# Optimization experiments

Hardware: AMD Instinct MI355X
Metric: run time of the kernel (lower is better)

The kernel has to match this reference:

```python
import jax, jax.numpy as jnp
import numpy as np

N = 100000   # nodes
E = 1600000  # edges
F = 64       # num_node_features
H = 48       # size_conv_layers
K = 5        # filter_size (Chebyshev order)
C = 2        # classes
EPS = 1e-5
SLOPE = 0.01  # LeakyReLU default negative_slope


def setup_inputs() -> dict:
    key = jax.random.key(0)
    ks = jax.random.split(key, 16)
    x = jax.random.normal(ks[0], (N, F), dtype=jnp.float32)
    edge_index = jax.random.randint(ks[1], (2, E), 0, N, dtype=jnp.int64)
    s = 0.1
    return {
        "x": x,
        "edge_index": edge_index,
        "W1": jax.random.normal(ks[2], (K, F, H), dtype=jnp.float32) * s,
        "b1": jnp.zeros((H,), jnp.float32),
        "W2": jax.random.normal(ks[3], (K, H, H), dtype=jnp.float32) * s,
        "b2": jnp.zeros((H,), jnp.float32),
        "W3": jax.random.normal(ks[4], (K, H, H), dtype=jnp.float32) * s,
        "b3": jnp.zeros((H,), jnp.float32),
        "g1": jnp.ones((H,), jnp.float32),
        "bt1": jnp.zeros((H,), jnp.float32),
        "g2": jnp.ones((H,), jnp.float32),
        "bt2": jnp.zeros((H,), jnp.float32),
        "Wf": jax.random.normal(ks[5], (H, C), dtype=jnp.float32) * s,
        "bf": jnp.zeros((C,), jnp.float32),
    }


def _cheb_norm(edge_index, n, dtype):
    # PyG ChebConv sym norm with lambda_max=2: L_hat = -D^-1/2 A D^-1/2 (zero diagonal)
    src, dst = edge_index[0], edge_index[1]
    deg = jax.ops.segment_sum(jnp.ones((edge_index.shape[1],), dtype), src, num_segments=n)
    dinv = jnp.where(deg > 0, jax.lax.rsqrt(jnp.maximum(deg, 1e-12)), 0.0)
    return -dinv[src] * dinv[dst], src, dst


def _cheb_conv(x, src, dst, norm, W, b, n):
    # Tx_0 = x; Tx_1 = L_hat x; Tx_k = 2 L_hat Tx_{k-1} - Tx_{k-2}
    def prop(t):
        return jax.ops.segment_sum(norm[:, None] * t[src], dst, num_segments=n)
    Tx0 = x
    out = Tx0 @ W[0]
    Tx1 = prop(Tx0)
    out = out + Tx1 @ W[1]
    for k in range(2, W.shape[0]):
        Tx2 = 2.0 * prop(Tx1) - Tx0
        out = out + Tx2 @ W[k]
        Tx0, Tx1 = Tx1, Tx2
    return out + b


def _bn_lrelu(x, g, b):
    mu = jnp.mean(x, axis=0)
    var = jnp.mean(jnp.square(x - mu), axis=0)  # biased var (train-mode BN)
    y = (x - mu) * jax.lax.rsqrt(var + EPS) * g + b
    return jnp.where(y >= 0, y, SLOPE * y)


def reference(x, edge_index, W1, b1, W2, b2, W3, b3, g1, bt1, g2, bt2, Wf, bf):
    n = x.shape[0]
    norm, src, dst = _cheb_norm(edge_index, n, x.dtype)
    h = _cheb_conv(x, src, dst, norm, W1, b1, n)
    h = _bn_lrelu(h, g1, bt1)
    h = _cheb_conv(h, src, dst, norm, W2, b2, n)
    h = _bn_lrelu(h, g2, bt2)
    h = _cheb_conv(h, src, dst, norm, W3, b3, n)  # no BN/act after last conv
    return h @ Wf + bf
```

## Files before the change

kernel.cpp:

```cpp
#include <hip/hip_runtime.h>

#define NHID 48
#define BN_EPS 1e-5f
#define SLOPE 0.01f
#define DMAX 64

typedef short short8 __attribute__((ext_vector_type(8)));
typedef float f32x4 __attribute__((ext_vector_type(4)));

__device__ __forceinline__ float bf_lo(unsigned u) { union { unsigned i; float f; } c; c.i = u << 16; return c.f; }
__device__ __forceinline__ float bf_hi(unsigned u) { union { unsigned i; float f; } c; c.i = u & 0xffff0000u; return c.f; }
__device__ __forceinline__ unsigned bf_rne(float x) { union { float f; unsigned i; } c; c.f = x; return (c.i + 0x7fffu + ((c.i >> 16) & 1u)) >> 16; }
__device__ __forceinline__ unsigned packbf(float lo, float hi) { return bf_rne(lo) | (bf_rne(hi) << 16); }

__device__ __forceinline__ void acc8(float (&a)[8], float w, const uint4& v) {
    a[0] = fmaf(w, bf_lo(v.x), a[0]); a[1] = fmaf(w, bf_hi(v.x), a[1]);
    a[2] = fmaf(w, bf_lo(v.y), a[2]); a[3] = fmaf(w, bf_hi(v.y), a[3]);
    a[4] = fmaf(w, bf_lo(v.z), a[4]); a[5] = fmaf(w, bf_hi(v.z), a[5]);
    a[6] = fmaf(w, bf_lo(v.w), a[6]); a[7] = fmaf(w, bf_hi(v.w), a[7]);
}

__global__ void k_setup(const int* __restrict__ src, const int* __restrict__ dst,
                        float* __restrict__ degf, int* __restrict__ cur,
                        int* __restrict__ csrc, int nE) {
    for (int e = blockIdx.x * blockDim.x + threadIdx.x; e < nE; e += gridDim.x * blockDim.x) {
        int s = src[e], d = dst[e];
        atomicAdd(&degf[s], 1.0f);
        int r = atomicAdd(&cur[d], 1);
        if (r < DMAX) csrc[(size_t)d * DMAX + r] = s;
    }
}

__global__ void k_dinv(float* __restrict__ deg, int nN) {
    for (int i = blockIdx.x * blockDim.x + threadIdx.x; i < nN; i += gridDim.x * blockDim.x) {
        float d = deg[i];
        deg[i] = (d > 0.f) ? rsqrtf(d) : 0.f;
    }
}

__global__ void k_cast(const float4* __restrict__ in, uint2* __restrict__ outv, int n4) {
    for (int i = blockIdx.x * blockDim.x + threadIdx.x; i < n4; i += gridDim.x * blockDim.x) {
        float4 v = in[i];
        outv[i] = make_uint2(packbf(v.x, v.y), packbf(v.z, v.w));
    }
}

template <int NV>
__global__ void k_prop(const uint4* __restrict__ Tin, const uint4* __restrict__ Tprev,
                       uint4* __restrict__ Tout, const int* __restrict__ cnt,
                       const int* __restrict__ csrc, const float* __restrict__ dinv,
                       int nN, int mode) {
    const int lane = threadIdx.x;
    const int x = lane & 7;
    const int y = lane >> 3;
    for (int n = blockIdx.x * 4 + threadIdx.y; n < nN; n += gridDim.x * 4) {
        int eb = n << 6;
        int c = cnt[n]; if (c > DMAX) c = DMAX;
        float a[8] = {0.f, 0.f, 0.f, 0.f, 0.f, 0.f, 0.f, 0.f};
        for (int it = 0; it < c; it += 16) {
            int j0 = it + y, j1 = it + 8 + y;
            int s0 = (j0 < c) ? csrc[eb + j0] : 0;
            int s1 = (j1 < c) ? csrc[eb + j1] : 0;
            float w0 = (j0 < c) ? dinv[s0] : 0.f;
            float w1 = (j1 < c) ? dinv[s1] : 0.f;
            if (x < NV) {
                uint4 q0 = Tin[(size_t)s0 * NV + x];
                uint4 q1 = Tin[(size_t)s1 * NV + x];
                acc8(a, w0, q0);
                acc8(a, w1, q1);
            }
        }
#pragma unroll
        for (int k = 0; k < 8; ++k) {
            float v = a[k];
            v += __shfl_xor(v, 8);
            v += __shfl_xor(v, 16);
            v += __shfl_xor(v, 32);
            a[k] = v;
        }
        if (y == 0 && x < NV) {
            float dn = -dinv[n];
            size_t o = (size_t)n * NV + x;
            uint4 r;
            if (mode) {
                uint4 p = Tprev[o];
                float t = 2.f * dn;
                r.x = packbf(fmaf(t, a[0], -bf_lo(p.x)), fmaf(t, a[1], -bf_hi(p.x)));
                r.y = packbf(fmaf(t, a[2], -bf_lo(p.y)), fmaf(t, a[3], -bf_hi(p.y)));
                r.z = packbf(fmaf(t, a[4], -bf_lo(p.z)), fmaf(t, a[5], -bf_hi(p.z)));
                r.w = packbf(fmaf(t, a[6], -bf_lo(p.w)), fmaf(t, a[7], -bf_hi(p.w)));
            } else {
                r.x = packbf(dn * a[0], dn * a[1]);
                r.y = packbf(dn * a[2], dn * a[3]);
                r.z = packbf(dn * a[4], dn * a[5]);
                r.w = packbf(dn * a[6], dn * a[7]);
            }
            Tout[o] = r;
        }
    }
}

template <int WIN, int MODE>
__global__ __launch_bounds__(256) void k_mmf(
    const unsigned short* __restrict__ Tslab, const float* __restrict__ Wb,
    const float* __restrict__ bias, unsigned short* __restrict__ Hout,
    float* __restrict__ bns, const float* __restrict__ Wf,
    const float* __restrict__ bfin, float* __restrict__ out, int nN) {
    constexpr int K = 5 * WIN;
    constexpr int NC = (K + 31) / 32;
    const int lane = threadIdx.x & 63;
    const int wid = threadIdx.x >> 6;
    const int col = lane & 15;
    const int sub = lane >> 4;
    const size_t termStride = (size_t)nN * WIN;

    short8 bfrag[3][NC];
#pragma unroll
    for (int ct = 0; ct < 3; ++ct) {
        int j = ct * 16 + col;
#pragma unroll
        for (int c = 0; c < NC; ++c) {
            short8 b;
#pragma unroll
            for (int r = 0; r < 8; ++r) {
                int k = c * 32 + sub * 8 + r;
                float w = (k < K) ? Wb[(size_t)k * 48 + j] : 0.f;
                b[r] = (short)bf_rne(w);
            }
            bfrag[ct][c] = b;
        }
    }
    float bj0 = bias[col], bj1 = bias[16 + col], bj2 = bias[32 + col];
    float wf00 = 0.f, wf01 = 0.f, wf02 = 0.f, wf10 = 0.f, wf11 = 0.f, wf12 = 0.f;
    float bf0 = 0.f, bf1 = 0.f;
    if (MODE == 1) {
        wf00 = Wf[(col) * 2 + 0];      wf10 = Wf[(col) * 2 + 1];
        wf01 = Wf[(16 + col) * 2 + 0]; wf11 = Wf[(16 + col) * 2 + 1];
        wf02 = Wf[(32 + col) * 2 + 0]; wf12 = Wf[(32 + col) * 2 + 1];
        bf0 = bfin[0]; bf1 = bfin[1];
    }
    float s0 = 0.f, s1 = 0.f, s2 = 0.f, q0 = 0.f, q1 = 0.f, q2 = 0.f;

    const int ntiles = (nN + 15) >> 4;
    for (int tile = blockIdx.x * 4 + wid; tile < ntiles; tile += gridDim.x * 4) {
        int n0 = tile << 4;
        int arow = n0 + col;
        bool rowok = arow < nN;
        f32x4 acc0 = {0.f, 0.f, 0.f, 0.f};
        f32x4 acc1 = {0.f, 0.f, 0.f, 0.f};
        f32x4 acc2 = {0.f, 0.f, 0.f, 0.f};
#pragma unroll
        for (int c = 0; c < NC; ++c) {
            int k = c * 32 + sub * 8;
            short8 a = {};
            if (rowok && k < K) {
                int t = k / WIN, f = k % WIN;
                a = *(const short8*)(Tslab + (size_t)t * termStride + (size_t)arow * WIN + f);
            }
            acc0 = __builtin_amdgcn_mfma_f32_16x16x32_bf16(a, bfrag[0][c], acc0, 0, 0, 0);
            acc1 = __builtin_amdgcn_mfma_f32_16x16x32_bf16(a, bfrag[1][c], acc1, 0, 0, 0);
            acc2 = __builtin_amdgcn_mfma_f32_16x16x32_bf16(a, bfrag[2][c], acc2, 0, 0, 0);
        }
        int nb = n0 + sub * 4;
        if (MODE == 0) {
#pragma unroll
            for (int r = 0; r < 4; ++r) {
                int n = nb + r;
                if (n < nN) {
                    float v0 = acc0[r] + bj0;
                    float v1 = acc1[r] + bj1;
                    float v2 = acc2[r] + bj2;
                    size_t ro = (size_t)n * NHID;
                    Hout[ro + col]      = (unsigned short)bf_rne(v0);
                    Hout[ro + 16 + col] = (unsigned short)bf_rne(v1);
                    Hout[ro + 32 + col] = (unsigned short)bf_rne(v2);
                    s0 += v0; q0 += v0 * v0;
                    s1 += v1; q1 += v1 * v1;
                    s2 += v2; q2 += v2 * v2;
                }
            }
        } else {
#pragma unroll
            for (int r = 0; r < 4; ++r) {
                float p0 = fmaf(acc0[r] + bj0, wf00, fmaf(acc1[r] + bj1, wf01, (acc2[r] + bj2) * wf02));
                float p1 = fmaf(acc0[r] + bj0, wf10, fmaf(acc1[r] + bj1, wf11, (acc2[r] + bj2) * wf12));
                p0 += __shfl_xor(p0, 1); p0 += __shfl_xor(p0, 2);
                p0 += __shfl_xor(p0, 4); p0 += __shfl_xor(p0, 8);
                p1 += __shfl_xor(p1, 1); p1 += __shfl_xor(p1, 2);
                p1 += __shfl_xor(p1, 4); p1 += __shfl_xor(p1, 8);
                int n = nb + r;
                if (col == 0 && n < nN) {
                    out[(size_t)n * 2 + 0] = p0 + bf0;
                    out[(size_t)n * 2 + 1] = p1 + bf1;
                }
            }
        }
    }
    if (MODE == 0) {
        s0 += __shfl_xor(s0, 16); s0 += __shfl_xor(s0, 32);
        s1 += __shfl_xor(s1, 16); s1 += __shfl_xor(s1, 32);
        s2 += __shfl_xor(s2, 16); s2 += __shfl_xor(s2, 32);
        q0 += __shfl_xor(q0, 16); q0 += __shfl_xor(q0, 32);
        q1 += __shfl_xor(q1, 16); q1 += __shfl_xor(q1, 32);
        q2 += __shfl_xor(q2, 16); q2 += __shfl_xor(q2, 32);
        __shared__ float red[4][96];
        if (lane < 16) {
            red[wid][col]      = s0; red[wid][16 + col] = s1; red[wid][32 + col] = s2;
            red[wid][48 + col] = q0; red[wid][64 + col] = q1; red[wid][80 + col] = q2;
        }
        __syncthreads();
        int t = threadIdx.x;
        if (t < 96) atomicAdd(&bns[t], red[0][t] + red[1][t] + red[2][t] + red[3][t]);
    }
}

__global__ void k_bn_apply(const unsigned short* __restrict__ Hin, unsigned short* __restrict__ T0,
                           const float* __restrict__ sums, const float* __restrict__ g,
                           const float* __restrict__ b, int nN) {
    int col = threadIdx.x;
    float inv = 1.f / (float)nN;
    float mu = sums[col] * inv;
    float var = sums[NHID + col] * inv - mu * mu;
    float rs = rsqrtf(var + BN_EPS) * g[col];
    float bb = b[col];
    for (int n = blockIdx.x * 8 + threadIdx.y; n < nN; n += gridDim.x * 8) {
        size_t o = (size_t)n * NHID + col;
        float y = (bf_lo(Hin[o]) - mu) * rs + bb;
        y = (y >= 0.f) ? y : SLOPE * y;
        T0[o] = (unsigned short)bf_rne(y);
    }
}

extern "C" void kernel_launch(void* const* d_in, const int* in_sizes, int n_in,
                              void* d_out, int out_size, void* d_ws, size_t ws_size,
                              hipStream_t stream) {
    const float* x   = (const float*)d_in[0];
    const int*   ei  = (const int*)d_in[1];
    const float* W1  = (const float*)d_in[2];
    const float* b1  = (const float*)d_in[3];
    const float* W2  = (const float*)d_in[4];
    const float* b2  = (const float*)d_in[5];
    const float* W3  = (const float*)d_in[6];
    const float* b3  = (const float*)d_in[7];
    const float* g1  = (const float*)d_in[8];
    const float* bt1 = (const float*)d_in[9];
    const float* g2  = (const float*)d_in[10];
    const float* bt2 = (const float*)d_in[11];
    const float* Wf  = (const float*)d_in[12];
    const float* bf  = (const float*)d_in[13];
    float* out = (float*)d_out;

    const int nN = in_sizes[0] / 64;
    const int nE = in_sizes[1] / 2;
    const int* src = ei;
    const int* dst = ei + nE;

    size_t off = 0;
    auto carve = [&](size_t bytes) -> void* {
        void* p = (char*)d_ws + off;
        off += (bytes + 255) & ~(size_t)255;
        return p;
    };
    float*          dinv = (float*)carve((size_t)nN * 4);
    int*            cur  = (int*)carve((size_t)nN * 4);
    int*            csrc = (int*)carve((size_t)nN * DMAX * 4);
    unsigned short* slab = (unsigned short*)carve((size_t)nN * 64 * 2 * 5);
    unsigned short* H    = (unsigned short*)carve((size_t)nN * NHID * 2);
    float*          bns  = (float*)carve(2 * NHID * 4);

    const size_t ts64 = (size_t)nN * 64;
    const size_t ts48 = (size_t)nN * NHID;

    hipMemsetAsync(dinv, 0, (size_t)nN * 4, stream);
    hipMemsetAsync(cur, 0, (size_t)nN * 4, stream);

    k_setup<<<4096, 256, 0, stream>>>(src, dst, dinv, cur, csrc, nE);
    k_dinv<<<1024, 256, 0, stream>>>(dinv, nN);
    k_cast<<<2048, 256, 0, stream>>>((const float4*)x, (uint2*)slab, nN * 16);

    const int gP = 2048;
    const dim3 blkP(64, 4);
    const int gM = 512;

    auto prop = [&](const unsigned short* Tin, const unsigned short* Tprev,
                    unsigned short* Tout, int NVw, int mode) {
        if (NVw == 8)
            k_prop<8><<<gP, blkP, 0, stream>>>((const uint4*)Tin, (const uint4*)Tprev,
                                               (uint4*)Tout, cur, csrc, dinv, nN, mode);
        else
            k_prop<6><<<gP, blkP, 0, stream>>>((const uint4*)Tin, (const uint4*)Tprev,
                                               (uint4*)Tout, cur, csrc, dinv, nN, mode);
    };

    unsigned short* L1[5];
    for (int t = 0; t < 5; ++t) L1[t] = slab + t * ts64;
    prop(L1[0], nullptr, L1[1], 8, 0);
    prop(L1[1], L1[0], L1[2], 8, 1);
    prop(L1[2], L1[1], L1[3], 8, 1);
    prop(L1[3], L1[2], L1[4], 8, 1);
    hipMemsetAsync(bns, 0, 2 * NHID * 4, stream);
    k_mmf<64, 0><<<gM, 256, 0, stream>>>(slab, W1, b1, H, bns, nullptr, nullptr, nullptr, nN);
    k_bn_apply<<<1024, dim3(NHID, 8), 0, stream>>>(H, slab, bns, g1, bt1, nN);

    unsigned short* L2[5];
    for (int t = 0; t < 5; ++t) L2[t] = slab + t * ts48;
    prop(L2[0], nullptr, L2[1], 6, 0);
    prop(L2[1], L2[0], L2[2], 6, 1);
    prop(L2[2], L2[1], L2[3], 6, 1);
    prop(L2[3], L2[2], L2[4], 6, 1);
    hipMemsetAsync(bns, 0, 2 * NHID * 4, stream);
    k_mmf<48, 0><<<gM, 256, 0, stream>>>(slab, W2, b2, H, bns, nullptr, nullptr, nullptr, nN);
    k_bn_apply<<<1024, dim3(NHID, 8), 0, stream>>>(H, slab, bns, g2, bt2, nN);

    prop(L2[0], nullptr, L2[1], 6, 0);
    prop(L2[1], L2[0], L2[2], 6, 1);
    prop(L2[2], L2[1], L2[3], 6, 1);
    prop(L2[3], L2[2], L2[4], 6, 1);
    k_mmf<48, 1><<<gM, 256, 0, stream>>>(slab, W3, b3, nullptr, nullptr, Wf, bf, out, nN);
}
```

Baseline: 813.9 us.

## Split feature slabs into 16-wide panels and propagate panel by panel

Stores each Chebyshev term as separate 16-feature panels (node-major within a panel) instead of full-width rows, and rewrites propagation to loop over panels, each edge gather reading 32 bytes per node from a smaller, more cache-resident panel. Matmul and BN-apply kernels are adapted to read and write the paneled layout, and the dinv and cast kernels are merged into one. The goal is better L2 locality for random neighbor gathers, at the cost of re-reading the CSR and dinv once per panel and using more shuffle reductions.

```diff
diff --git a/kernel.cpp b/kernel.cpp
--- a/kernel.cpp
+++ b/kernel.cpp
@@ -31,71 +31,75 @@
     }
 }
 
-__global__ void k_dinv(float* __restrict__ deg, int nN) {
-    for (int i = blockIdx.x * blockDim.x + threadIdx.x; i < nN; i += gridDim.x * blockDim.x) {
+__global__ void k_dinvcast(float* __restrict__ deg, int nN,
+                           const float4* __restrict__ xin, uint2* __restrict__ outv, int n4) {
+    int stride = gridDim.x * blockDim.x;
+    int gid = blockIdx.x * blockDim.x + threadIdx.x;
+    for (int i = gid; i < n4; i += stride) {
+        float4 v = xin[i];
+        int n = i >> 4, q = i & 15;
+        int p = q >> 2, w = q & 3;
+        outv[((size_t)p * nN + n) * 4 + w] = make_uint2(packbf(v.x, v.y), packbf(v.z, v.w));
+    }
+    for (int i = gid; i < nN; i += stride) {
         float d = deg[i];
         deg[i] = (d > 0.f) ? rsqrtf(d) : 0.f;
     }
 }
 
-__global__ void k_cast(const float4* __restrict__ in, uint2* __restrict__ outv, int n4) {
-    for (int i = blockIdx.x * blockDim.x + threadIdx.x; i < n4; i += gridDim.x * blockDim.x) {
-        float4 v = in[i];
-        outv[i] = make_uint2(packbf(v.x, v.y), packbf(v.z, v.w));
-    }
-}
-
-template <int NV>
-__global__ void k_prop(const uint4* __restrict__ Tin, const uint4* __restrict__ Tprev,
-                       uint4* __restrict__ Tout, const int* __restrict__ cnt,
-                       const int* __restrict__ csrc, const float* __restrict__ dinv,
-                       int nN, int mode) {
+__global__ void k_propP(const unsigned short* __restrict__ Tin,
+                        const unsigned short* __restrict__ Tprev,
+                        unsigned short* __restrict__ Tout,
+                        const int* __restrict__ cnt, const int* __restrict__ csrc,
+                        const float* __restrict__ dinv, int nN, int NP, int mode) {
     const int lane = threadIdx.x;
-    const int x = lane & 7;
-    const int y = lane >> 3;
-    for (int n = blockIdx.x * 4 + threadIdx.y; n < nN; n += gridDim.x * 4) {
-        int eb = n << 6;
-        int c = cnt[n]; if (c > DMAX) c = DMAX;
-        float a[8] = {0.f, 0.f, 0.f, 0.f, 0.f, 0.f, 0.f, 0.f};
-        for (int it = 0; it < c; it += 16) {
-            int j0 = it + y, j1 = it + 8 + y;
-            int s0 = (j0 < c) ? csrc[eb + j0] : 0;
-            int s1 = (j1 < c) ? csrc[eb + j1] : 0;
-            float w0 = (j0 < c) ? dinv[s0] : 0.f;
-            float w1 = (j1 < c) ? dinv[s1] : 0.f;
-            if (x < NV) {
-                uint4 q0 = Tin[(size_t)s0 * NV + x];
-                uint4 q1 = Tin[(size_t)s1 * NV + x];
-                acc8(a, w0, q0);
-                acc8(a, w1, q1);
-            }
-        }
-#pragma unroll
-        for (int k = 0; k < 8; ++k) {
-            float v = a[k];
-            v += __shfl_xor(v, 8);
-            v += __shfl_xor(v, 16);
-            v += __shfl_xor(v, 32);
-            a[k] = v;
-        }
-        if (y == 0 && x < NV) {
-            float dn = -dinv[n];
-            size_t o = (size_t)n * NV + x;
-            uint4 r;
-            if (mode) {
-                uint4 p = Tprev[o];
-                float t = 2.f * dn;
-                r.x = packbf(fmaf(t, a[0], -bf_lo(p.x)), fmaf(t, a[1], -bf_hi(p.x)));
-                r.y = packbf(fmaf(t, a[2], -bf_lo(p.y)), fmaf(t, a[3], -bf_hi(p.y)));
-                r.z = packbf(fmaf(t, a[4], -bf_lo(p.z)), fmaf(t, a[5], -bf_hi(p.z)));
-                r.w = packbf(fmaf(t, a[6], -bf_lo(p.w)), fmaf(t, a[7], -bf_hi(p.w)));
-            } else {
-                r.x = packbf(dn * a[0], dn * a[1]);
-                r.y = packbf(dn * a[2], dn * a[3]);
-                r.z = packbf(dn * a[4], dn * a[5]);
-                r.w = packbf(dn * a[6], dn * a[7]);
-            }
-            Tout[o] = r;
+    const int x = lane & 1;
+    const int y = (lane >> 1) & 15;
+    const int z = lane >> 5;
+    const size_t S = (size_t)nN * 16;
+    for (int p = 0; p < NP; ++p) {
+        const uint4* tin = (const uint4*)(Tin + p * S);
+        const uint4* tpv = (const uint4*)(Tprev + p * S);
+        uint4* tout = (uint4*)(Tout + p * S);
+        for (int n = blockIdx.x * 8 + threadIdx.y * 2 + z; n < nN; n += gridDim.x * 8) {
+            int eb = n << 6;
+            int c = cnt[n]; if (c > DMAX) c = DMAX;
+            float a[8] = {0.f, 0.f, 0.f, 0.f, 0.f, 0.f, 0.f, 0.f};
+            for (int it = 0; it < c; it += 16) {
+                int j = it + y;
+                int s = (j < c) ? csrc[eb + j] : 0;
+                float w = (j < c) ? dinv[s] : 0.f;
+                uint4 q = tin[(size_t)s * 2 + x];
+                acc8(a, w, q);
+            }
+#pragma unroll
+            for (int k = 0; k < 8; ++k) {
+                float v = a[k];
+                v += __shfl_xor(v, 2);
+                v += __shfl_xor(v, 4);
+                v += __shfl_xor(v, 8);
+                v += __shfl_xor(v, 16);
+                a[k] = v;
+            }
+            if (y == 0) {
+                float dn = -dinv[n];
+                size_t o = (size_t)n * 2 + x;
+                uint4 r;
+                if (mode) {
+                    uint4 pv = tpv[o];
+                    float t = 2.f * dn;
+                    r.x = packbf(fmaf(t, a[0], -bf_lo(pv.x)), fmaf(t, a[1], -bf_hi(pv.x)));
+                    r.y = packbf(fmaf(t, a[2], -bf_lo(pv.y)), fmaf(t, a[3], -bf_hi(pv.y)));
+                    r.z = packbf(fmaf(t, a[4], -bf_lo(pv.z)), fmaf(t, a[5], -bf_hi(pv.z)));
+                    r.w = packbf(fmaf(t, a[6], -bf_lo(pv.w)), fmaf(t, a[7], -bf_hi(pv.w)));
+                } else {
+                    r.x = packbf(dn * a[0], dn * a[1]);
+                    r.y = packbf(dn * a[2], dn * a[3]);
+                    r.z = packbf(dn * a[4], dn * a[5]);
+                    r.w = packbf(dn * a[6], dn * a[7]);
+                }
+                tout[o] = r;
+            }
         }
     }
 }
@@ -108,11 +112,13 @@
     const float* __restrict__ bfin, float* __restrict__ out, int nN) {
     constexpr int K = 5 * WIN;
     constexpr int NC = (K + 31) / 32;
+    constexpr int PMAX = K / 16;
     const int lane = threadIdx.x & 63;
     const int wid = threadIdx.x >> 6;
     const int col = lane & 15;
     const int sub = lane >> 4;
-    const size_t termStride = (size_t)nN * WIN;
+    const int hs = sub >> 1;
+    const size_t S = (size_t)nN * 16;
 
     short8 bfrag[3][NC];
 #pragma unroll
@@ -151,11 +157,10 @@
         f32x4 acc2 = {0.f, 0.f, 0.f, 0.f};
 #pragma unroll
         for (int c = 0; c < NC; ++c) {
-            int k = c * 32 + sub * 8;
+            int pp = 2 * c + hs;
             short8 a = {};
-            if (rowok && k < K) {
-                int t = k / WIN, f = k % WIN;
-                a = *(const short8*)(Tslab + (size_t)t * termStride + (size_t)arow * WIN + f);
+            if (rowok && pp < PMAX) {
+                a = *(const short8*)(Tslab + (size_t)pp * S + (size_t)arow * 16 + (sub & 1) * 8);
             }
             acc0 = __builtin_amdgcn_mfma_f32_16x16x32_bf16(a, bfrag[0][c], acc0, 0, 0, 0);
             acc1 = __builtin_amdgcn_mfma_f32_16x16x32_bf16(a, bfrag[1][c], acc1, 0, 0, 0);
@@ -223,11 +228,11 @@
     float var = sums[NHID + col] * inv - mu * mu;
     float rs = rsqrtf(var + BN_EPS) * g[col];
     float bb = b[col];
+    size_t pbase = (size_t)(col >> 4) * (size_t)nN * 16 + (col & 15);
     for (int n = blockIdx.x * 8 + threadIdx.y; n < nN; n += gridDim.x * 8) {
-        size_t o = (size_t)n * NHID + col;
-        float y = (bf_lo(Hin[o]) - mu) * rs + bb;
+        float y = (bf_lo(Hin[(size_t)n * NHID + col]) - mu) * rs + bb;
         y = (y >= 0.f) ? y : SLOPE * y;
-        T0[o] = (unsigned short)bf_rne(y);
+        T0[pbase + (size_t)n * 16] = (unsigned short)bf_rne(y);
     }
 }
 
@@ -275,46 +280,40 @@
     hipMemsetAsync(cur, 0, (size_t)nN * 4, stream);
 
     k_setup<<<4096, 256, 0, stream>>>(src, dst, dinv, cur, csrc, nE);
-    k_dinv<<<1024, 256, 0, stream>>>(dinv, nN);
-    k_cast<<<2048, 256, 0, stream>>>((const float4*)x, (uint2*)slab, nN * 16);
+    k_dinvcast<<<2048, 256, 0, stream>>>(dinv, nN, (const float4*)x, (uint2*)slab, nN * 16);
 
     const int gP = 2048;
     const dim3 blkP(64, 4);
     const int gM = 512;
 
     auto prop = [&](const unsigned short* Tin, const unsigned short* Tprev,
-                    unsigned short* Tout, int NVw, int mode) {
-        if (NVw == 8)
-            k_prop<8><<<gP, blkP, 0, stream>>>((const uint4*)Tin, (const uint4*)Tprev,
-                                               (uint4*)Tout, cur, csrc, dinv, nN, mode);
-        else
-            k_prop<6><<<gP, blkP, 0, stream>>>((const uint4*)Tin, (const uint4*)Tprev,
-                                               (uint4*)Tout, cur, csrc, dinv, nN, mode);
+                    unsigned short* Tout, int NP, int mode) {
+        k_propP<<<gP, blkP, 0, stream>>>(Tin, Tprev ? Tprev : Tin, Tout, cur, csrc, dinv, nN, NP, mode);
     };
 
     unsigned short* L1[5];
     for (int t = 0; t < 5; ++t) L1[t] = slab + t * ts64;
-    prop(L1[0], nullptr, L1[1], 8, 0);
-    prop(L1[1], L1[0], L1[2], 8, 1);
-    prop(L1[2], L1[1], L1[3], 8, 1);
-    prop(L1[3], L1[2], L1[4], 8, 1);
+    prop(L1[0], nullptr, L1[1], 4, 0);
+    prop(L1[1], L1[0], L1[2], 4, 1);
+    prop(L1[2], L1[1], L1[3], 4, 1);
+    prop(L1[3], L1[2], L1[4], 4, 1);
     hipMemsetAsync(bns, 0, 2 * NHID * 4, stream);
     k_mmf<64, 0><<<gM, 256, 0, stream>>>(slab, W1, b1, H, bns, nullptr, nullptr, nullptr, nN);
     k_bn_apply<<<1024, dim3(NHID, 8), 0, stream>>>(H, slab, bns, g1, bt1, nN);
 
     unsigned short* L2[5];
     for (int t = 0; t < 5; ++t) L2[t] = slab + t * ts48;
-    prop(L2[0], nullptr, L2[1], 6, 0);
-    prop(L2[1], L2[0], L2[2], 6, 1);
-    prop(L2[2], L2[1], L2[3], 6, 1);
-    prop(L2[3], L2[2], L2[4], 6, 1);
+    prop(L2[0], nullptr, L2[1], 3, 0);
+    prop(L2[1], L2[0], L2[2], 3, 1);
+    prop(L2[2], L2[1], L2[3], 3, 1);
+    prop(L2[3], L2[2], L2[4], 3, 1);
     hipMemsetAsync(bns, 0, 2 * NHID * 4, stream);
     k_mmf<48, 0><<<gM, 256, 0, stream>>>(slab, W2, b2, H, bns, nullptr, nullptr, nullptr, nN);
     k_bn_apply<<<1024, dim3(NHID, 8), 0, stream>>>(H, slab, bns, g2, bt2, nN);
 
-    prop(L2[0], nullptr, L2[1], 6, 0);
-    prop(L2[1], L2[0], L2[2], 6, 1);
-    prop(L2[2], L2[1], L2[3], 6, 1);
-    prop(L2[3], L2[2], L2[4], 6, 1);
+    prop(L2[0], nullptr, L2[1], 3, 0);
+    prop(L2[1], L2[0], L2[2], 3, 1);
+    prop(L2[2], L2[1], L2[3], 3, 1);
+    prop(L2[3], L2[2], L2[4], 3, 1);
     k_mmf<48, 1><<<gM, 256, 0, stream>>>(slab, W3, b3, nullptr, nullptr, Wf, bf, out, nN);
 }
```

After: 1.201 ms. 47.6% more time.
